# Kernel optimization log

Measured on AMD Instinct MI355X. Metric: run time of the kernel, lower is better.

Reference implementation:

```python
import jax, jax.numpy as jnp
import numpy as np

L, K, D, V, S, B = 2, 4, 1024, 32000, 1024, 2

# Constant neighbor influence from the 2x2 grid (success_rate==0.5 for fresh blocks)
_pos = np.array([[0, 0], [0, 1], [1, 0], [1, 1]], dtype=np.float64)
_dist = np.sqrt(((_pos[:, None, :] - _pos[None, :, :]) ** 2).sum(-1))
_infl = np.where(np.eye(K, dtype=bool), 0.0, 0.5 / (1.0 + _dist)).sum(-1)
NEIGHBOR_SIG = jnp.asarray(1.0 / (1.0 + np.exp(-_infl)), dtype=jnp.float32)  # [K]


def _ln(x, g, b, eps=1e-5):
    mu = x.mean(-1, keepdims=True)
    var = ((x - mu) ** 2).mean(-1, keepdims=True)
    return (x - mu) / jnp.sqrt(var + eps) * g + b


def setup_inputs() -> dict:
    key = jax.random.key(0)
    ks = jax.random.split(key, 10)
    def n(k, shape, s):
        return jax.random.normal(k, shape, jnp.float32) * s
    return {
        "input_ids": jax.random.randint(ks[0], (B, S), 0, V),
        "embedding": n(ks[1], (V, D), 0.02),
        "pos_enc": n(ks[2], (S, D), 0.02),
        "torsion_field": jnp.zeros((D,), jnp.float32),
        "ln1_g": jnp.ones((L, D), jnp.float32),
        "ln1_b": jnp.zeros((L, D), jnp.float32),
        "base_W": n(ks[3], (L, D, D), 0.02),
        "blk_W1": n(ks[4], (L, K, D // 2, D), 0.02),
        "blk_W2": n(ks[5], (L, K, D, D // 2), 0.02),
        "blk_gate": n(ks[6], (L, K, D), 0.01),
        "prop_W": n(ks[7], (L, K, K), 0.5),
        "prop_b": jnp.zeros((L, K), jnp.float32),
        "ln2_g": jnp.ones((L, D), jnp.float32),
        "ln2_b": jnp.zeros((L, D), jnp.float32),
        "out_ln_g": jnp.ones((D,), jnp.float32),
        "out_ln_b": jnp.zeros((D,), jnp.float32),
        "lm_head_W": n(ks[8], (V, D), 0.02),
    }


def reference(input_ids, embedding, pos_enc, torsion_field, ln1_g, ln1_b,
              base_W, blk_W1, blk_W2, blk_gate, prop_W, prop_b,
              ln2_g, ln2_b, out_ln_g, out_ln_b, lm_head_W):
    h = embedding[input_ids] + pos_enc[None]  # [B,S,D]
    s = jnp.full((K,), 0.5, h.dtype)  # fresh blocks: success_rate = 0.5
    for l in range(L):
        # excitement (detached in torch via .item())
        exc0 = jax.nn.sigmoid(prop_W[l] @ s + prop_b[l])
        exc = jax.lax.stop_gradient(0.6 * exc0 + 0.4 * NEIGHBOR_SIG)  # [K]
        hn = _ln(h, ln1_g[l], ln1_b[l])
        base = hn @ base_W[l].T  # [B,S,D]
        # all K blocks are always loaded (min_blocks == max_blocks == 4)
        t = jnp.einsum('bsd,khd->bksh', hn, blk_W1[l])
        t = jax.nn.gelu(t, approximate=False)
        t = jnp.einsum('bksh,kdh->bksd', t, blk_W2[l])
        gate = jax.nn.sigmoid(blk_gate[l] + torsion_field)  # [K,D]
        t = t * gate[None, :, None, :]
        combined = jnp.einsum('bksd,k->bsd', t, exc) / exc.sum()
        h = h + (base + combined) * 0.3
        h = _ln(h, ln2_g[l], ln2_b[l])
    h = _ln(h, out_ln_g, out_ln_b)
    return h @ lm_head_W.T  # [B,S,V]
```

## Files before the change

### kernel.cpp

```cpp
#include <hip/hip_runtime.h>
#include <math.h>

typedef unsigned short u16;
typedef short s16x8 __attribute__((ext_vector_type(8)));
typedef float f32x4 __attribute__((ext_vector_type(4)));
typedef u16 u16x4 __attribute__((ext_vector_type(4)));
typedef int i32x4 __attribute__((ext_vector_type(4)));

#define D 1024
#define MM 2048
#define HH 512
#define VV 32000

static __device__ __forceinline__ u16 f2bf(float f) {
    union { float f; unsigned int i; } c; c.f = f;
    unsigned int x = c.i;
    return (u16)((x + 0x7fffu + ((x >> 16) & 1u)) >> 16);
}
static __device__ __forceinline__ float sigm(float x) { return 1.0f / (1.0f + expf(-x)); }

static __device__ __forceinline__ void load_lds16(const u16* g, u16* l) {
    __builtin_amdgcn_global_load_lds(
        (const __attribute__((address_space(1))) unsigned int*)g,
        (__attribute__((address_space(3))) unsigned int*)l, 16, 0, 0);
}

__global__ __launch_bounds__(256) void cvt_kernel(const float* __restrict__ in,
                                                  u16* __restrict__ out, const int n4)
{
    for (int i = blockIdx.x * 256 + threadIdx.x; i < n4; i += gridDim.x * 256) {
        f32x4 v = ((const f32x4*)in)[i];
        u16x4 o;
#pragma unroll
        for (int j = 0; j < 4; j++) o[j] = f2bf(v[j]);
        ((u16x4*)out)[i] = o;
    }
}

__global__ __launch_bounds__(256) void embed_kernel(const int* __restrict__ ids,
    const float* __restrict__ emb, const float* __restrict__ pos, float* __restrict__ h)
{
    const int m = blockIdx.x;
    const int s = m & 1023;
    const long id = ids[m];
    const int d = threadIdx.x * 4;
    f32x4 ev = *(const f32x4*)&emb[id * D + d];
    f32x4 pv = *(const f32x4*)&pos[(long)s * D + d];
    f32x4 o;
#pragma unroll
    for (int i = 0; i < 4; i++) o[i] = ev[i] + pv[i];
    *(f32x4*)&h[(long)m * D + d] = o;
}

__global__ __launch_bounds__(256) void ln_bf16_kernel(const float* __restrict__ h,
    u16* __restrict__ out, const float* __restrict__ g, const float* __restrict__ b)
{
    const int row = blockIdx.x;
    const int d = threadIdx.x * 4;
    f32x4 x = *(const f32x4*)&h[(long)row * D + d];
    float s = x[0] + x[1] + x[2] + x[3];
    float ss = x[0]*x[0] + x[1]*x[1] + x[2]*x[2] + x[3]*x[3];
#pragma unroll
    for (int off = 32; off; off >>= 1) { s += __shfl_xor(s, off); ss += __shfl_xor(ss, off); }
    __shared__ float red[8];
    const int wid = threadIdx.x >> 6;
    if ((threadIdx.x & 63) == 0) { red[wid] = s; red[4 + wid] = ss; }
    __syncthreads();
    s = red[0] + red[1] + red[2] + red[3];
    ss = red[4] + red[5] + red[6] + red[7];
    const float mu = s * (1.0f / D);
    const float rstd = rsqrtf(ss * (1.0f / D) - mu * mu + 1e-5f);
    f32x4 gv = *(const f32x4*)&g[d];
    f32x4 bv = *(const f32x4*)&b[d];
    u16x4 o;
#pragma unroll
    for (int i = 0; i < 4; i++) o[i] = f2bf((x[i] - mu) * rstd * gv[i] + bv[i]);
    *(u16x4*)&out[(long)row * D + d] = o;
}

__global__ __launch_bounds__(256) void resln_kernel(float* __restrict__ h,
    const float* __restrict__ c, const float* __restrict__ g, const float* __restrict__ b)
{
    const int row = blockIdx.x;
    const int d = threadIdx.x * 4;
    f32x4 x = *(const f32x4*)&h[(long)row * D + d];
    f32x4 cv = *(const f32x4*)&c[(long)row * D + d];
#pragma unroll
    for (int i = 0; i < 4; i++) x[i] += 0.3f * cv[i];
    float s = x[0] + x[1] + x[2] + x[3];
    float ss = x[0]*x[0] + x[1]*x[1] + x[2]*x[2] + x[3]*x[3];
#pragma unroll
    for (int off = 32; off; off >>= 1) { s += __shfl_xor(s, off); ss += __shfl_xor(ss, off); }
    __shared__ float red[8];
    const int wid = threadIdx.x >> 6;
    if ((threadIdx.x & 63) == 0) { red[wid] = s; red[4 + wid] = ss; }
    __syncthreads();
    s = red[0] + red[1] + red[2] + red[3];
    ss = red[4] + red[5] + red[6] + red[7];
    const float mu = s * (1.0f / D);
    const float rstd = rsqrtf(ss * (1.0f / D) - mu * mu + 1e-5f);
    f32x4 gv = *(const f32x4*)&g[d];
    f32x4 bv = *(const f32x4*)&b[d];
    f32x4 o;
#pragma unroll
    for (int i = 0; i < 4; i++) o[i] = (x[i] - mu) * rstd * gv[i] + bv[i];
    *(f32x4*)&h[(long)row * D + d] = o;
}

__global__ void exc_kernel(const float* __restrict__ pW, const float* __restrict__ pb,
                           float* __restrict__ sc)
{
    if (threadIdx.x == 0 && blockIdx.x == 0) {
        const float NS = 1.0f / (1.0f + expf(-0.70710678118654752f));
        float e[4], sum = 0.0f;
        for (int k = 0; k < 4; k++) {
            float a = pb[k];
            for (int j = 0; j < 4; j++) a += 0.5f * pW[k * 4 + j];
            e[k] = 0.6f * sigm(a) + 0.4f * NS;
            sum += e[k];
        }
        for (int k = 0; k < 4; k++) sc[k] = e[k] / sum;
    }
}

__global__ __launch_bounds__(256) void scale_w2_kernel(
    const float* __restrict__ W2l, const float* __restrict__ gatel,
    const float* __restrict__ tors, const float* __restrict__ sc,
    u16* __restrict__ W2eff)
{
    const int n = blockIdx.x >> 1;
    const int half = blockIdx.x & 1;
    const int kh = half * 1024 + threadIdx.x * 4;
    const int k = kh >> 9;
    const int hh = kh & 511;
    const float f = sigm(gatel[k * D + n] + tors[n]) * sc[k];
    f32x4 w = *(const f32x4*)&W2l[((long)k * D + n) * HH + hh];
    u16x4 o;
#pragma unroll
    for (int i = 0; i < 4; i++) o[i] = f2bf(w[i] * f);
    *(u16x4*)&W2eff[(long)n * 2048 + kh] = o;
}

template<int EPI, int BN>
__global__ __launch_bounds__(256) void gemm_lds_kernel(
    const u16* __restrict__ A, const u16* __restrict__ W,
    float* __restrict__ Cf, u16* __restrict__ Cb,
    const int K, const long ldc, const long strideWz, const long strideCz)
{
    W += (long)blockIdx.z * strideWz;
    if (EPI == 1) Cb += (long)blockIdx.z * strideCz;
    else          Cf += (long)blockIdx.z * strideCz;

    const int gx = gridDim.x;
    const int nwg = gx * gridDim.y;
    int lin = blockIdx.y * gx + blockIdx.x;
    lin = (lin & 7) * (nwg >> 3) + (lin >> 3);
    const int bm = (lin % gx) * 128;
    const int bn = (lin / gx) * BN;

    __shared__ __align__(16) u16 As[128 * 32];
    __shared__ __align__(16) u16 Bs[BN * 32];

    const int tid = threadIdx.x;
    const int lane = tid & 63;
    const int w = tid >> 6;
    const int wm = (w >> 1) * 64;
    const int wn = (w & 1) * (BN / 2);
    const int lr = lane & 15;
    const int lkb = (lane >> 4) * 16;

    const int srow = lane >> 2;
    const int scol = (lane & 3) * 8;

    constexpr int NA = 8;
    constexpr int NB = BN / 16;
    constexpr int NIT = (NA + NB) / 4;

    f32x4 acc[4][BN / 32];
#pragma unroll
    for (int i = 0; i < 4; i++)
#pragma unroll
        for (int j = 0; j < BN / 32; j++) acc[i][j] = f32x4{0.f, 0.f, 0.f, 0.f};

    for (int k0 = 0; k0 < K; k0 += 32) {
        __syncthreads();
#pragma unroll
        for (int it = 0; it < NIT; ++it) {
            const int c = w + it * 4;
            if (c < NA) {
                load_lds16(&A[(long)(bm + c * 16 + srow) * K + k0 + scol], &As[c * 512]);
            } else {
                const int c2 = c - NA;
                load_lds16(&W[(long)(bn + c2 * 16 + srow) * K + k0 + scol], &Bs[c2 * 512]);
            }
        }
        __syncthreads();
        s16x8 a[4], b[BN / 32];
#pragma unroll
        for (int i = 0; i < 4; i++)
            a[i] = *(const s16x8*)((const char*)As + (wm + i * 16 + lr) * 64 + lkb);
#pragma unroll
        for (int j = 0; j < BN / 32; j++)
            b[j] = *(const s16x8*)((const char*)Bs + (wn + j * 16 + lr) * 64 + lkb);
#pragma unroll
        for (int i = 0; i < 4; i++)
#pragma unroll
            for (int j = 0; j < BN / 32; j++)
                acc[i][j] = __builtin_amdgcn_mfma_f32_16x16x32_bf16(a[i], b[j], acc[i][j], 0, 0, 0);
    }

    const int r0 = (lane >> 4) * 4;
#pragma unroll
    for (int i = 0; i < 4; i++) {
#pragma unroll
        for (int j = 0; j < BN / 32; j++) {
            const int n = bn + wn + j * 16 + lr;
#pragma unroll
            for (int r = 0; r < 4; r++) {
                const int m = bm + wm + i * 16 + r0 + r;
                const float v = acc[i][j][r];
                if (EPI == 0) {
                    Cf[(long)m * ldc + n] = v;
                } else if (EPI == 1) {
                    const float gel = 0.5f * v * (1.0f + erff(v * 0.70710678118654752f));
                    Cb[(long)m * ldc + n] = f2bf(gel);
                } else {
                    Cf[(long)m * ldc + n] += v;
                }
            }
        }
    }
}


#define AU16  16384
#define HALFU 8192
#define BB0   32768

#define BAR() do { __builtin_amdgcn_s_barrier(); __builtin_amdgcn_sched_barrier(0); } while (0)

__global__ __launch_bounds__(512, 2) void gemm256_kernel(
    const u16* __restrict__ Ag, const u16* __restrict__ Wg, float* __restrict__ C)
{
    __shared__ __align__(16) u16 lds[65536];

    const int nwg = gridDim.x * gridDim.y;
    int lin = blockIdx.y * gridDim.x + blockIdx.x;
    lin = (lin & 7) * (nwg >> 3) + (lin >> 3);
    const int bm = (lin & 7) * 256;
    const int bn = (lin >> 3) * 256;

    const int tid = threadIdx.x;
    const int lane = tid & 63;
    const int w = tid >> 6;
    const int wm = w >> 2;
    const int wn = w & 3;

    const u16* aSrc = Ag + (long)(bm + w * 16 + (lane & 15)) * 1024 + ((lane >> 4) * 8);
    const u16* bSrc = Wg + (long)(bn + w * 16 + (lane & 15)) * 1024 + ((lane >> 4) * 8);
    u16* aDst = lds + w * 1024;
    u16* bDst = lds + BB0 + w * 1024;

    auto stageA = [&](int kt, int b, int kk) {
        const long co = (long)kt * 64 + kk * 32;
        load_lds16(aSrc + co,               aDst + b * AU16 + kk * 512);
        load_lds16(aSrc + co + 128 * 1024L, aDst + b * AU16 + HALFU + kk * 512);
    };
    auto stageB = [&](int kt, int b, int kk) {
        const long co = (long)kt * 64 + kk * 32;
        load_lds16(bSrc + co,               bDst + b * AU16 + kk * 512);
        load_lds16(bSrc + co + 128 * 1024L, bDst + b * AU16 + HALFU + kk * 512);
    };

    const u16* aRd = lds + wm * HALFU + lane * 8;
    const u16* bRd = lds + BB0 + (wn >> 1) * HALFU + (wn & 1) * 4096 + lane * 8;

    f32x4 acc[8][4];
#pragma unroll
    for (int i = 0; i < 8; ++i)
#pragma unroll
        for (int j = 0; j < 4; ++j) acc[i][j] = f32x4{0.f, 0.f, 0.f, 0.f};

    stageA(0, 0, 0); stageB(0, 0, 0); stageA(0, 0, 1); stageB(0, 0, 1);
    stageA(1, 1, 0); stageB(1, 1, 0); stageA(1, 1, 1);
    asm volatile("s_waitcnt vmcnt(6)" ::: "memory");
    BAR();

    auto ktile = [&](int t, int b) {
        const int t1 = (t + 1) & 15, t2 = (t + 2) & 15;
        s16x8 af[8], bf[2];
#pragma unroll
        for (int i = 0; i < 8; ++i) af[i] = *(const s16x8*)(aRd + b * AU16 + i * 1024);
#pragma unroll
        for (int j = 0; j < 2; ++j) bf[j] = *(const s16x8*)(bRd + b * AU16 + j * 1024);
        stageB(t1, b ^ 1, 1);
        BAR();
        __builtin_amdgcn_s_setprio(1);
#pragma unroll
        for (int i = 0; i < 8; ++i) {
            acc[i][0] = __builtin_amdgcn_mfma_f32_16x16x32_bf16(af[i], bf[0], acc[i][0], 0, 0, 0);
            acc[i][1] = __builtin_amdgcn_mfma_f32_16x16x32_bf16(af[i], bf[1], acc[i][1], 0, 0, 0);
        }
        __builtin_amdgcn_s_setprio(0);
        BAR();
#pragma unroll
        for (int j = 0; j < 2; ++j) bf[j] = *(const s16x8*)(bRd + b * AU16 + 2048 + j * 1024);
        stageA(t2, b, 0);
        BAR();
        __builtin_amdgcn_s_setprio(1);
#pragma unroll
        for (int i = 0; i < 8; ++i) {
            acc[i][2] = __builtin_amdgcn_mfma_f32_16x16x32_bf16(af[i], bf[0], acc[i][2], 0, 0, 0);
            acc[i][3] = __builtin_amdgcn_mfma_f32_16x16x32_bf16(af[i], bf[1], acc[i][3], 0, 0, 0);
        }
        __builtin_amdgcn_s_setprio(0);
        BAR();
#pragma unroll
        for (int i = 0; i < 8; ++i) af[i] = *(const s16x8*)(aRd + b * AU16 + i * 1024 + 512);
#pragma unroll
        for (int j = 0; j < 2; ++j) bf[j] = *(const s16x8*)(bRd + b * AU16 + j * 1024 + 512);
        stageB(t2, b, 0);
        BAR();
        __builtin_amdgcn_s_setprio(1);
#pragma unroll
        for (int i = 0; i < 8; ++i) {
            acc[i][0] = __builtin_amdgcn_mfma_f32_16x16x32_bf16(af[i], bf[0], acc[i][0], 0, 0, 0);
            acc[i][1] = __builtin_amdgcn_mfma_f32_16x16x32_bf16(af[i], bf[1], acc[i][1], 0, 0, 0);
        }
        __builtin_amdgcn_s_setprio(0);
        BAR();
#pragma unroll
        for (int j = 0; j < 2; ++j) bf[j] = *(const s16x8*)(bRd + b * AU16 + 2048 + j * 1024 + 512);
        stageA(t2, b, 1);
        BAR();
        __builtin_amdgcn_s_setprio(1);
#pragma unroll
        for (int i = 0; i < 8; ++i) {
            acc[i][2] = __builtin_amdgcn_mfma_f32_16x16x32_bf16(af[i], bf[0], acc[i][2], 0, 0, 0);
            acc[i][3] = __builtin_amdgcn_mfma_f32_16x16x32_bf16(af[i], bf[1], acc[i][3], 0, 0, 0);
        }
        __builtin_amdgcn_s_setprio(0);
        asm volatile("s_waitcnt vmcnt(6)" ::: "memory");
        BAR();
    };

    for (int tt = 0; tt < 8; ++tt) {
        ktile(2 * tt,     0);
        ktile(2 * tt + 1, 1);
    }

    asm volatile("s_waitcnt vmcnt(0)" ::: "memory");

    const int r0 = (lane >> 4) * 4;
    const int cl = lane & 15;
#pragma unroll
    for (int i = 0; i < 8; ++i)
#pragma unroll
        for (int j = 0; j < 4; ++j) {
            const long m = bm + wm * 128 + i * 16 + r0;
            const int n = bn + wn * 64 + j * 16 + cl;
#pragma unroll
            for (int rr = 0; rr < 4; ++rr)
                C[(m + rr) * (long)VV + n] = acc[i][j][rr];
        }
}

extern "C" void kernel_launch(void* const* d_in, const int* in_sizes, int n_in,
                              void* d_out, int out_size, void* d_ws, size_t ws_size,
                              hipStream_t stream)
{
    (void)in_sizes; (void)n_in; (void)out_size; (void)ws_size;
    const int*   ids   = (const int*)d_in[0];
    const float* emb   = (const float*)d_in[1];
    const float* pos   = (const float*)d_in[2];
    const float* tors  = (const float*)d_in[3];
    const float* ln1g  = (const float*)d_in[4];
    const float* ln1b  = (const float*)d_in[5];
    const float* baseW = (const float*)d_in[6];
    const float* W1    = (const float*)d_in[7];
    const float* W2    = (const float*)d_in[8];
    const float* gate  = (const float*)d_in[9];
    const float* propW = (const float*)d_in[10];
    const float* propb = (const float*)d_in[11];
    const float* ln2g  = (const float*)d_in[12];
    const float* ln2b  = (const float*)d_in[13];
    const float* outg  = (const float*)d_in[14];
    const float* outb  = (const float*)d_in[15];
    const float* lmW   = (const float*)d_in[16];

    char* ws = (char*)d_ws;
    float* h     = (float*)(ws);
    u16*   hn    = (u16*)  (ws + (8l  << 20));
    u16*   bWbf  = (u16*)  (ws + (12l << 20));
    u16*   W1bf  = (u16*)  (ws + (14l << 20));
    float* C     = (float*)(ws + (18l << 20));
    u16*   t     = (u16*)  (ws + (26l << 20));
    u16*   W2eff = (u16*)  (ws + (34l << 20));
    float* sc    = (float*)(ws + (38l << 20));
    u16*   lmWbf = (u16*)  (ws + (12l << 20));

    embed_kernel<<<MM, 256, 0, stream>>>(ids, emb, pos, h);

    for (int l = 0; l < 2; l++) {
        exc_kernel<<<1, 64, 0, stream>>>(propW + l * 16, propb + l * 4, sc);
        ln_bf16_kernel<<<MM, 256, 0, stream>>>(h, hn, ln1g + (long)l * D, ln1b + (long)l * D);
        cvt_kernel<<<1024, 256, 0, stream>>>(baseW + (long)l * D * D, bWbf, D * D / 4);
        cvt_kernel<<<2048, 256, 0, stream>>>(W1 + (long)l * 4 * HH * D, W1bf, 4 * HH * D / 4);
        gemm_lds_kernel<0, 64><<<dim3(16, 16, 1), 256, 0, stream>>>(
            hn, bWbf, C, nullptr, D, D, 0, 0);
        gemm_lds_kernel<1, 64><<<dim3(16, 8, 4), 256, 0, stream>>>(
            hn, W1bf, nullptr, t, D, 2048, (long)HH * D, 512);
        scale_w2_kernel<<<2048, 256, 0, stream>>>(
            W2 + (long)l * 4 * D * HH, gate + (long)l * 4 * D, tors, sc, W2eff);
        gemm_lds_kernel<2, 64><<<dim3(16, 16, 1), 256, 0, stream>>>(
            t, W2eff, C, nullptr, 2048, D, 0, 0);
        resln_kernel<<<MM, 256, 0, stream>>>(h, C, ln2g + (long)l * D, ln2b + (long)l * D);
    }

    ln_bf16_kernel<<<MM, 256, 0, stream>>>(h, hn, outg, outb);
    cvt_kernel<<<2048, 256, 0, stream>>>(lmW, lmWbf, VV * D / 4);
    gemm256_kernel<<<dim3(8, 125), 512, 0, stream>>>(hn, lmWbf, (float*)d_out);
}
```

Before: 442.8 us.

## Restructure LM-head GEMM main loop into register double-buffered phases with fewer barriers

Replaces the four-subphase ktile loop, which had a barrier around every MFMA group, with 32 half-k-tile phases. Each phase prefetches the next phase's A and B fragments from LDS into a second register set, issues one A+B global-to-LDS stage, runs 32 MFMAs, and then takes a single wait plus barrier. The aim is to cut barrier count and hide LDS read latency behind MFMA work. In exchange it doubles the fragment registers, which risks spills at 2 blocks per CU, and the LDS buffer reuse timing becomes more delicate.

```diff
diff --git a/kernel.cpp b/kernel.cpp
--- a/kernel.cpp
+++ b/kernel.cpp
@@ -237,8 +237,6 @@
 #define HALFU 8192
 #define BB0   32768
 
-#define BAR() do { __builtin_amdgcn_s_barrier(); __builtin_amdgcn_sched_barrier(0); } while (0)
-
 __global__ __launch_bounds__(512, 2) void gemm256_kernel(
     const u16* __restrict__ Ag, const u16* __restrict__ Wg, float* __restrict__ C)
 {
@@ -281,72 +279,50 @@
 #pragma unroll
         for (int j = 0; j < 4; ++j) acc[i][j] = f32x4{0.f, 0.f, 0.f, 0.f};
 
-    stageA(0, 0, 0); stageB(0, 0, 0); stageA(0, 0, 1); stageB(0, 0, 1);
-    stageA(1, 1, 0); stageB(1, 1, 0); stageA(1, 1, 1);
-    asm volatile("s_waitcnt vmcnt(6)" ::: "memory");
-    BAR();
-
-    auto ktile = [&](int t, int b) {
-        const int t1 = (t + 1) & 15, t2 = (t + 2) & 15;
-        s16x8 af[8], bf[2];
-#pragma unroll
-        for (int i = 0; i < 8; ++i) af[i] = *(const s16x8*)(aRd + b * AU16 + i * 1024);
-#pragma unroll
-        for (int j = 0; j < 2; ++j) bf[j] = *(const s16x8*)(bRd + b * AU16 + j * 1024);
-        stageB(t1, b ^ 1, 1);
-        BAR();
+    s16x8 F0[12], F1[12];
+
+    stageA(0, 0, 0); stageB(0, 0, 0);
+    stageA(0, 0, 1); stageB(0, 0, 1);
+    stageA(1, 1, 0); stageB(1, 1, 0);
+    asm volatile("s_waitcnt vmcnt(4)" ::: "memory");
+    __builtin_amdgcn_s_barrier();
+    __builtin_amdgcn_sched_barrier(0);
+
+#pragma unroll
+    for (int i = 0; i < 8; ++i) F0[i] = *(const s16x8*)(aRd + i * 1024);
+#pragma unroll
+    for (int j = 0; j < 4; ++j) F0[8 + j] = *(const s16x8*)(bRd + j * 1024);
+
+    auto phase = [&](int p, s16x8 (&fu)[12], s16x8 (&fl)[12]) {
+        const int pr = p + 1;
+        const int Tr = (pr >> 1) & 15, kkr = pr & 1, br = Tr & 1;
+        const u16* aR = aRd + br * AU16 + kkr * 512;
+        const u16* bR = bRd + br * AU16 + kkr * 512;
+#pragma unroll
+        for (int i = 0; i < 8; ++i) fl[i] = *(const s16x8*)(aR + i * 1024);
+#pragma unroll
+        for (int j = 0; j < 4; ++j) fl[8 + j] = *(const s16x8*)(bR + j * 1024);
+        const int us = 6 + 2 * p;
+        const int Ts = (us >> 2) & 15, kks = (us >> 1) & 1, bs = Ts & 1;
+        stageA(Ts, bs, kks);
+        stageB(Ts, bs, kks);
+        __builtin_amdgcn_sched_barrier(0);
         __builtin_amdgcn_s_setprio(1);
 #pragma unroll
-        for (int i = 0; i < 8; ++i) {
-            acc[i][0] = __builtin_amdgcn_mfma_f32_16x16x32_bf16(af[i], bf[0], acc[i][0], 0, 0, 0);
-            acc[i][1] = __builtin_amdgcn_mfma_f32_16x16x32_bf16(af[i], bf[1], acc[i][1], 0, 0, 0);
-        }
+        for (int j = 0; j < 4; ++j)
+#pragma unroll
+            for (int i = 0; i < 8; ++i)
+                acc[i][j] = __builtin_amdgcn_mfma_f32_16x16x32_bf16(fu[i], fu[8 + j], acc[i][j], 0, 0, 0);
         __builtin_amdgcn_s_setprio(0);
-        BAR();
-#pragma unroll
-        for (int j = 0; j < 2; ++j) bf[j] = *(const s16x8*)(bRd + b * AU16 + 2048 + j * 1024);
-        stageA(t2, b, 0);
-        BAR();
-        __builtin_amdgcn_s_setprio(1);
-#pragma unroll
-        for (int i = 0; i < 8; ++i) {
-            acc[i][2] = __builtin_amdgcn_mfma_f32_16x16x32_bf16(af[i], bf[0], acc[i][2], 0, 0, 0);
-            acc[i][3] = __builtin_amdgcn_mfma_f32_16x16x32_bf16(af[i], bf[1], acc[i][3], 0, 0, 0);
-        }
-        __builtin_amdgcn_s_setprio(0);
-        BAR();
-#pragma unroll
-        for (int i = 0; i < 8; ++i) af[i] = *(const s16x8*)(aRd + b * AU16 + i * 1024 + 512);
-#pragma unroll
-        for (int j = 0; j < 2; ++j) bf[j] = *(const s16x8*)(bRd + b * AU16 + j * 1024 + 512);
-        stageB(t2, b, 0);
-        BAR();
-        __builtin_amdgcn_s_setprio(1);
-#pragma unroll
-        for (int i = 0; i < 8; ++i) {
-            acc[i][0] = __builtin_amdgcn_mfma_f32_16x16x32_bf16(af[i], bf[0], acc[i][0], 0, 0, 0);
-            acc[i][1] = __builtin_amdgcn_mfma_f32_16x16x32_bf16(af[i], bf[1], acc[i][1], 0, 0, 0);
-        }
-        __builtin_amdgcn_s_setprio(0);
-        BAR();
-#pragma unroll
-        for (int j = 0; j < 2; ++j) bf[j] = *(const s16x8*)(bRd + b * AU16 + 2048 + j * 1024 + 512);
-        stageA(t2, b, 1);
-        BAR();
-        __builtin_amdgcn_s_setprio(1);
-#pragma unroll
-        for (int i = 0; i < 8; ++i) {
-            acc[i][2] = __builtin_amdgcn_mfma_f32_16x16x32_bf16(af[i], bf[0], acc[i][2], 0, 0, 0);
-            acc[i][3] = __builtin_amdgcn_mfma_f32_16x16x32_bf16(af[i], bf[1], acc[i][3], 0, 0, 0);
-        }
-        __builtin_amdgcn_s_setprio(0);
-        asm volatile("s_waitcnt vmcnt(6)" ::: "memory");
-        BAR();
+        __builtin_amdgcn_sched_barrier(0);
+        asm volatile("s_waitcnt vmcnt(4)" ::: "memory");
+        __builtin_amdgcn_s_barrier();
+        __builtin_amdgcn_sched_barrier(0);
     };
 
-    for (int tt = 0; tt < 8; ++tt) {
-        ktile(2 * tt,     0);
-        ktile(2 * tt + 1, 1);
+    for (int p = 0; p < 32; p += 2) {
+        phase(p,     F0, F1);
+        phase(p + 1, F1, F0);
     }
 
     asm volatile("s_waitcnt vmcnt(0)" ::: "memory");
```

Result: no change. 441.9 us (-0.2%).
